# Kernel tuning notes

Measured on AMD Instinct MI355X. Metric: run time of the kernel, lower is better.

Reference implementation:

```python
import jax, jax.numpy as jnp
import numpy as np

C = 128
K = 5
M = 150000   # num vertices
NF = 300000  # num faces
D = 192      # volume side
NEG_SLOPE = 0.2


def _x_shift(K):
    # Exactly replicates the torch module's grid construction.
    grid = np.linspace(-K // 2, K // 2, K)
    grid_3d = np.stack(np.meshgrid(grid, grid, grid), axis=0).transpose(2, 1, 3, 0)
    return jnp.asarray(grid_3d.reshape(-1, 3), jnp.float32)  # [K^3, 3]


def _trilinear_border(vol, g):
    # vol: [D1, D2, D3]; g: [N, 3] normalized coords in (x, y, z) order
    # (x -> D3/W, y -> D2/H, z -> D1/D), align_corners=True, padding_mode='border'.
    D1, D2, D3 = vol.shape
    def pix(c, S):
        return jnp.clip((c + 1.0) * 0.5 * (S - 1), 0.0, S - 1.0)
    ix, iy, iz = pix(g[:, 0], D3), pix(g[:, 1], D2), pix(g[:, 2], D1)
    x0f, y0f, z0f = jnp.floor(ix), jnp.floor(iy), jnp.floor(iz)
    wx, wy, wz = ix - x0f, iy - y0f, iz - z0f
    x0 = x0f.astype(jnp.int32); y0 = y0f.astype(jnp.int32); z0 = z0f.astype(jnp.int32)
    x1 = jnp.minimum(x0 + 1, D3 - 1)
    y1 = jnp.minimum(y0 + 1, D2 - 1)
    z1 = jnp.minimum(z0 + 1, D1 - 1)
    c000 = vol[z0, y0, x0]; c001 = vol[z0, y0, x1]
    c010 = vol[z0, y1, x0]; c011 = vol[z0, y1, x1]
    c100 = vol[z1, y0, x0]; c101 = vol[z1, y0, x1]
    c110 = vol[z1, y1, x0]; c111 = vol[z1, y1, x1]
    c00 = c000 * (1 - wx) + c001 * wx
    c01 = c010 * (1 - wx) + c011 * wx
    c10 = c100 * (1 - wx) + c101 * wx
    c11 = c110 * (1 - wx) + c111 * wx
    c0 = c00 * (1 - wy) + c01 * wy
    c1 = c10 * (1 - wy) + c11 * wy
    return c0 * (1 - wz) + c1 * wz


def _leaky(x):
    return jnp.where(x >= 0, x, NEG_SLOPE * x)


def setup_inputs() -> dict:
    key = jax.random.key(0)
    ks = jax.random.split(key, 9)
    v = jax.random.uniform(ks[0], (1, M, 3), jnp.float32, -0.9, 0.9)
    f = jax.random.randint(ks[1], (1, NF, 3), 0, M, jnp.int32)
    V = jax.random.normal(ks[2], (1, 1, D, D, D), jnp.float32)
    def init(k, shape, fan):
        return jax.random.normal(k, shape, jnp.float32) / np.sqrt(fan).astype(np.float32)
    Wconv = init(ks[3], (C, 1, K, K, K), K ** 3)
    bconv = jnp.zeros((C,), jnp.float32)
    Wlfc = init(ks[4], (C, C), C)
    blfc = jnp.zeros((C,), jnp.float32)
    W1 = init(ks[5], (C, 6), 6)
    b1 = jnp.zeros((C,), jnp.float32)
    W2 = init(ks[6], (4 * C, 2 * C), 2 * C)
    b2 = jnp.zeros((4 * C,), jnp.float32)
    W3 = init(ks[7], (2 * C, 4 * C), 4 * C)
    b3 = jnp.zeros((2 * C,), jnp.float32)
    return dict(v=v, f=f, V=V, Wconv=Wconv, bconv=bconv, Wlfc=Wlfc, blfc=blfc,
                W1=W1, b1=b1, W2=W2, b2=b2, W3=W3, b3=b3)


def reference(v, f, V, Wconv, bconv, Wlfc, blfc, W1, b1, W2, b2, W3, b3):
    m = v.shape[1]
    D1, D2, D3 = V.shape[2], V.shape[3], V.shape[4]
    Dm = max(D1, D2, D3)
    rescale = jnp.array([D3 / Dm, D2 / Dm, D1 / Dm], jnp.float32)
    x_shift = _x_shift(K)  # [K^3, 3]

    # --- cube sampling (Q = n_scale = 1), done under no_grad in torch ---
    pts = (v[0][:, None, :] + x_shift / Dm * 2.0) / rescale  # [m, K^3, 3]
    cubes = _trilinear_border(V[0, 0], pts.reshape(-1, 3)).reshape(m, K ** 3)
    cubes = jax.lax.stop_gradient(cubes)

    # --- localconv: Conv3d with full-size kernel == GEMM over flattened cube ---
    z_local = cubes @ Wconv.reshape(C, -1).T + bconv      # [m, C]
    z_local = _leaky(z_local)
    z_local = _leaky(z_local @ Wlfc.T + blfc)             # [m, C]

    # --- vertex normals (area-weighted face-normal accumulation, pytorch3d style) ---
    faces = f[0]
    vv = v[0]
    p0, p1, p2 = vv[faces[:, 0]], vv[faces[:, 1]], vv[faces[:, 2]]
    fn = jnp.cross(p1 - p0, p2 - p0)
    vn = jnp.zeros_like(vv)
    vn = vn.at[faces[:, 0]].add(fn).at[faces[:, 1]].add(fn).at[faces[:, 2]].add(fn)
    vn = vn / jnp.maximum(jnp.linalg.norm(vn, axis=-1, keepdims=True), 1e-6)

    # --- point-wise MLP fusion ---
    x = jnp.concatenate([v, vn[None]], axis=2)            # [1, m, 6]
    z_point = _leaky(x @ W1.T + b1)                       # [1, m, C]
    z = jnp.concatenate([z_point, z_local[None]], axis=2) # [1, m, 2C]
    z = _leaky(z @ W2.T + b2)                             # [1, m, 4C]
    z = _leaky(z @ W3.T + b3)                             # [1, m, 2C]
    return z
```

## Files before the change

kernel.cpp:

```cpp
#include <hip/hip_runtime.h>
#include <hip/hip_fp16.h>

#define NEG_SLOPE 0.2f

using f16x8 = __attribute__((ext_vector_type(8))) _Float16;
using f32x4 = __attribute__((ext_vector_type(4))) float;

__device__ __forceinline__ float leakyf(float x) { return x >= 0.f ? x : NEG_SLOPE * x; }

__device__ __forceinline__ void gload_lds16(const void* g, void* l) {
    __builtin_amdgcn_global_load_lds(
        (const __attribute__((address_space(1))) unsigned int*)g,
        (__attribute__((address_space(3))) unsigned int*)l, 16, 0, 0);
}

#define MFMA16(a, b, c) __builtin_amdgcn_mfma_f32_16x16x32_f16(a, b, c, 0, 0, 0)

__global__ __launch_bounds__(256)
void normals_kernel(const float* __restrict__ v, const int* __restrict__ f,
                    float* __restrict__ vn, int nf) {
    int i = blockIdx.x * 256 + threadIdx.x;
    if (i >= nf) return;
    int i0 = f[3 * i], i1 = f[3 * i + 1], i2 = f[3 * i + 2];
    float p0x = v[3 * i0], p0y = v[3 * i0 + 1], p0z = v[3 * i0 + 2];
    float ux = v[3 * i1] - p0x, uy = v[3 * i1 + 1] - p0y, uz = v[3 * i1 + 2] - p0z;
    float wx = v[3 * i2] - p0x, wy = v[3 * i2 + 1] - p0y, wz = v[3 * i2 + 2] - p0z;
    float fx = uy * wz - uz * wy;
    float fy = uz * wx - ux * wz;
    float fz = ux * wy - uy * wx;
    atomicAdd(&vn[3 * i0 + 0], fx); atomicAdd(&vn[3 * i0 + 1], fy); atomicAdd(&vn[3 * i0 + 2], fz);
    atomicAdd(&vn[3 * i1 + 0], fx); atomicAdd(&vn[3 * i1 + 1], fy); atomicAdd(&vn[3 * i1 + 2], fz);
    atomicAdd(&vn[3 * i2 + 0], fx); atomicAdd(&vn[3 * i2 + 1], fy); atomicAdd(&vn[3 * i2 + 2], fz);
}

__global__ __launch_bounds__(256)
void code_hist_kernel(const float* __restrict__ v, int* __restrict__ codes,
                      int* __restrict__ hist, int M) {
    int i = blockIdx.x * 256 + threadIdx.x;
    if (i >= M) return;
    int cx = min(max((int)((v[3 * i + 0] + 1.f) * 8.f), 0), 15);
    int cy = min(max((int)((v[3 * i + 1] + 1.f) * 8.f), 0), 15);
    int cz = min(max((int)((v[3 * i + 2] + 1.f) * 8.f), 0), 15);
    int code = 0;
#pragma unroll
    for (int b = 0; b < 4; ++b)
        code |= (((cx >> b) & 1) << (3 * b)) | (((cy >> b) & 1) << (3 * b + 1)) |
                (((cz >> b) & 1) << (3 * b + 2));
    codes[i] = code;
    atomicAdd(&hist[code], 1);
}

__global__ __launch_bounds__(1024)
void scan_kernel(const int* __restrict__ hist, int* __restrict__ offs) {
    __shared__ int s[1024];
    int t = threadIdx.x;
    int v0 = hist[4 * t], v1 = hist[4 * t + 1], v2 = hist[4 * t + 2], v3 = hist[4 * t + 3];
    int sum = v0 + v1 + v2 + v3;
    s[t] = sum;
    __syncthreads();
    for (int d = 1; d < 1024; d <<= 1) {
        int val = (t >= d) ? s[t - d] : 0;
        __syncthreads();
        s[t] += val;
        __syncthreads();
    }
    int excl = s[t] - sum;
    offs[4 * t + 0] = excl;
    offs[4 * t + 1] = excl + v0;
    offs[4 * t + 2] = excl + v0 + v1;
    offs[4 * t + 3] = excl + v0 + v1 + v2;
}

__global__ __launch_bounds__(256)
void scatter_kernel(const int* __restrict__ codes, int* __restrict__ offs,
                    int* __restrict__ perm, int M) {
    int i = blockIdx.x * 256 + threadIdx.x;
    if (i >= M) return;
    int pos = atomicAdd(&offs[codes[i]], 1);
    perm[pos] = i;
}

__global__ __launch_bounds__(256)
void sample_kernel(const float* __restrict__ v, const float* __restrict__ vol,
                   const int* __restrict__ perm,
                   __half* __restrict__ cubes, int m_start, int cnt, int nwg) {
    __shared__ float bbox[2][392];
    __shared__ int pi0[2][16];
    __shared__ float pw[2][16];
    const int half = threadIdx.x >> 7;
    const int q = threadIdx.x & 127;
    int q8 = nwg >> 3, r8 = nwg & 7;
    int xcd = blockIdx.x & 7, idxb = blockIdx.x >> 3;
    int bid = (xcd < r8 ? xcd * (q8 + 1) : r8 * (q8 + 1) + (xcd - r8) * q8) + idxb;
    int ml = bid * 2 + half;
    bool valid = ml < cnt;
    int m = valid ? perm[m_start + ml] : 0;

    if (valid && q < 15) {
        int axis = q / 5, idx = q - 5 * axis;
        float g = -3.f + 1.25f * (float)idx;
        float p = v[3 * m + axis] + g / 192.f * 2.f;
        float pos = fminf(fmaxf((p + 1.f) * 0.5f * 191.f, 0.f), 191.f);
        float fl = floorf(pos);
        pi0[half][q] = (int)fl;
        pw[half][q] = pos - fl;
    }
    __syncthreads();
    if (valid) {
        int xlo = pi0[half][0], ylo = pi0[half][5], zlo = pi0[half][10];
        for (int i = q; i < 392; i += 128) {
            int dx = i & 7;
            int dy = (i >> 3) % 7;
            int dz = i / 56;
            int X = min(xlo + dx, 191), Y = min(ylo + dy, 191), Z = min(zlo + dz, 191);
            bbox[half][i] = vol[Z * 36864 + Y * 192 + X];
        }
    }
    __syncthreads();
    if (!valid) return;
    __half* dst = cubes + (size_t)ml * 128;
    if (q >= 125) { dst[q] = __float2half(0.f); return; }
    int a = q % 5, b = (q / 5) % 5, c = q / 25;
    int xlo = pi0[half][0], ylo = pi0[half][5], zlo = pi0[half][10];
    int gx0 = pi0[half][a], gy0 = pi0[half][5 + b], gz0 = pi0[half][10 + c];
    float wxv = pw[half][a], wyv = pw[half][5 + b], wzv = pw[half][10 + c];
    int x0 = gx0 - xlo, y0 = gy0 - ylo, z0 = gz0 - zlo;
    int x1 = min(gx0 + 1, 191) - xlo;
    int y1 = min(gy0 + 1, 191) - ylo;
    int z1 = min(gz0 + 1, 191) - zlo;
    const float* bb = bbox[half];
    int b00 = (z0 * 7 + y0) * 8, b01 = (z0 * 7 + y1) * 8;
    int b10 = (z1 * 7 + y0) * 8, b11 = (z1 * 7 + y1) * 8;
    float c000 = bb[b00 + x0], c001 = bb[b00 + x1];
    float c010 = bb[b01 + x0], c011 = bb[b01 + x1];
    float c100 = bb[b10 + x0], c101 = bb[b10 + x1];
    float c110 = bb[b11 + x0], c111 = bb[b11 + x1];
    float omx = 1.f - wxv, omy = 1.f - wyv, omz = 1.f - wzv;
    float c00 = c000 * omx + c001 * wxv;
    float c01 = c010 * omx + c011 * wxv;
    float c10 = c100 * omx + c101 * wxv;
    float c11 = c110 * omx + c111 * wxv;
    float c0 = c00 * omy + c01 * wyv;
    float c1 = c10 * omy + c11 * wyv;
    dst[25 * a + 5 * b + c] = __float2half(c0 * omz + c1 * wzv);
}

__global__ __launch_bounds__(256)
void prep_weights(const float* __restrict__ Wconv, const float* __restrict__ Wlfc,
                  const float* __restrict__ W2, const float* __restrict__ W3,
                  __half* __restrict__ wpadh, __half* __restrict__ wlfch,
                  __half* __restrict__ w2h, __half* __restrict__ w3h) {
    int b = blockIdx.x, t = threadIdx.x;
    if (b < 64) {
        int i = b * 256 + t; int ch = i >> 7, k = i & 127;
        wpadh[i] = __float2half(k < 125 ? Wconv[ch * 125 + k] : 0.f);
    } else if (b < 128) {
        int i = (b - 64) * 256 + t; wlfch[i] = __float2half(Wlfc[i]);
    } else if (b < 640) {
        int i = (b - 128) * 256 + t; w2h[i] = __float2half(W2[i]);
    } else {
        int i = (b - 640) * 256 + t; w3h[i] = __float2half(W3[i]);
    }
}

__global__ __launch_bounds__(256)
void point_kernel(const float* __restrict__ v, const float* __restrict__ vn,
                  const int* __restrict__ perm,
                  const float* __restrict__ W1, const float* __restrict__ b1,
                  __half* __restrict__ zcat, int m_start, int cnt) {
    int ml = blockIdx.x * 2 + (threadIdx.x >> 7);
    if (ml >= cnt) return;
    int n = threadIdx.x & 127;
    int m = perm[m_start + ml];
    float x0 = v[3 * m], x1 = v[3 * m + 1], x2 = v[3 * m + 2];
    float nx = vn[3 * m], ny = vn[3 * m + 1], nz = vn[3 * m + 2];
    float nrm = fmaxf(sqrtf(nx * nx + ny * ny + nz * nz), 1e-6f);
    nx /= nrm; ny /= nrm; nz /= nrm;
    const float* w = W1 + n * 6;
    float z = b1[n] + x0 * w[0] + x1 * w[1] + x2 * w[2] + nx * w[3] + ny * w[4] + nz * w[5];
    zcat[(size_t)ml * 256 + n] = __float2half(leakyf(z));
}

__global__ __launch_bounds__(256)
void convlfc_kernel(const __half* __restrict__ cubes, const __half* __restrict__ wconvh,
                    const float* __restrict__ bconv, const __half* __restrict__ wlfch,
                    const float* __restrict__ blfc, __half* __restrict__ zcat) {
    __shared__ __half Zt[128 * 128];
    __shared__ __half As[128 * 64];
    __shared__ __half Bs[128 * 64];
    const int t = threadIdx.x;
    const int lane = t & 63, wave = t >> 6;
    const int lr = lane & 15, lg = lane >> 4;
    const int wm = wave >> 1, wn = wave & 1;
    const int m0 = blockIdx.x * 128;
    const int srow = t >> 3;
    const int scb = ((t & 7) << 4) ^ (((t >> 3) & 7) << 4);
    const int swz = (lr & 7) << 4;

    const __half* Ag = cubes + (size_t)(m0 + srow) * 128 + (scb >> 1);
    const __half* Bg = wconvh + (size_t)srow * 128 + (scb >> 1);
    __half* Al = As + wave * 512;
    __half* Bl = Bs + wave * 512;
    const char* aB = (const char*)As + (wm * 64 + lr) * 128;
    const char* bB = (const char*)Bs + (wn * 64 + lr) * 128;

    f32x4 acc[4][4] = {};
    for (int kc = 0; kc < 128; kc += 64) {
#pragma unroll
        for (int i = 0; i < 4; ++i) {
            gload_lds16(Ag + (size_t)i * 32 * 128 + kc, Al + i * 2048);
            gload_lds16(Bg + (size_t)i * 32 * 128 + kc, Bl + i * 2048);
        }
        __syncthreads();
#pragma unroll
        for (int kk = 0; kk < 2; ++kk) {
            const int ko = (kk * 64 + lg * 16) ^ swz;
            f16x8 af[4], bf[4];
#pragma unroll
            for (int fx = 0; fx < 4; ++fx) {
                af[fx] = *(const f16x8*)(aB + fx * 2048 + ko);
                bf[fx] = *(const f16x8*)(bB + fx * 2048 + ko);
            }
#pragma unroll
            for (int fm = 0; fm < 4; ++fm)
#pragma unroll
                for (int fn = 0; fn < 4; ++fn)
                    acc[fm][fn] = MFMA16(af[fm], bf[fn], acc[fm][fn]);
        }
        __syncthreads();
    }
#pragma unroll
    for (int fm = 0; fm < 4; ++fm) {
#pragma unroll
        for (int fn = 0; fn < 4; ++fn) {
            int col = wn * 64 + fn * 16 + lr;
            float bias = bconv[col];
#pragma unroll
            for (int r = 0; r < 4; ++r) {
                int row = wm * 64 + fm * 16 + lg * 4 + r;
                float val = leakyf(acc[fm][fn][r] + bias);
                *(__half*)((char*)Zt + row * 256 + ((2 * col) ^ ((row & 7) << 4))) = __float2half(val);
            }
        }
    }
    __syncthreads();

    const __half* Bg2 = wlfch + (size_t)srow * 128 + (scb >> 1);
    const char* zR = (const char*)Zt + (wm * 64 + lr) * 256;
    f32x4 acc2[4][4] = {};
    for (int kc = 0; kc < 128; kc += 64) {
#pragma unroll
        for (int i = 0; i < 4; ++i)
            gload_lds16(Bg2 + (size_t)i * 32 * 128 + kc, Bl + i * 2048);
        __syncthreads();
#pragma unroll
        for (int kk = 0; kk < 2; ++kk) {
            const int kb = kc * 2 + kk * 64 + lg * 16;
            const int ko = (kk * 64 + lg * 16) ^ swz;
            f16x8 af[4], bf[4];
#pragma unroll
            for (int fx = 0; fx < 4; ++fx) {
                af[fx] = *(const f16x8*)(zR + fx * 4096 + (kb ^ swz));
                bf[fx] = *(const f16x8*)(bB + fx * 2048 + ko);
            }
#pragma unroll
            for (int fm = 0; fm < 4; ++fm)
#pragma unroll
                for (int fn = 0; fn < 4; ++fn)
                    acc2[fm][fn] = MFMA16(af[fm], bf[fn], acc2[fm][fn]);
        }
        __syncthreads();
    }
#pragma unroll
    for (int fm = 0; fm < 4; ++fm) {
#pragma unroll
        for (int fn = 0; fn < 4; ++fn) {
            int col = wn * 64 + fn * 16 + lr;
            float bias = blfc[col];
#pragma unroll
            for (int r = 0; r < 4; ++r) {
                int row = m0 + wm * 64 + fm * 16 + lg * 4 + r;
                zcat[(size_t)row * 256 + 128 + col] = __float2half(leakyf(acc2[fm][fn][r] + bias));
            }
        }
    }
}

template<bool F32OUT>
__global__ __launch_bounds__(256)
void gemm_mfma(const __half* __restrict__ A, const __half* __restrict__ W,
               const float* __restrict__ bias, void* __restrict__ outp,
               int K, int Meff, int OS, int OC, const int* __restrict__ rowmap) {
    __shared__ __half As[8192];
    __shared__ __half Bs[8192];
    const int t = threadIdx.x;
    const int lane = t & 63, wave = t >> 6;
    const int lr = lane & 15, lg = lane >> 4;
    const int wm = wave >> 1, wn = wave & 1;
    const int m0 = blockIdx.x * 128, n0 = blockIdx.y * 128;

    const int srow = t >> 3;
    const int scb = ((t & 7) << 4) ^ (((t >> 3) & 7) << 4);
    const __half* Ag = A + (size_t)(m0 + srow) * K + (scb >> 1);
    const __half* Wg = W + (size_t)(n0 + srow) * K + (scb >> 1);
    __half* Al = As + wave * 512;
    __half* Bl = Bs + wave * 512;

    const int swz = (lr & 7) << 4;
    const char* aB = (const char*)As + (wm * 64 + lr) * 128;
    const char* bB = (const char*)Bs + (wn * 64 + lr) * 128;
    const int k0 = (lg * 16) ^ swz;
    const int k1 = (64 + lg * 16) ^ swz;

    f32x4 acc[4][4] = {};

    for (int kc = 0; kc < K; kc += 64) {
#pragma unroll
        for (int i = 0; i < 4; ++i) {
            gload_lds16(Ag + (size_t)i * 32 * K + kc, Al + i * 2048);
            gload_lds16(Wg + (size_t)i * 32 * K + kc, Bl + i * 2048);
        }
        __syncthreads();
        f16x8 af[4], bf[4];
#pragma unroll
        for (int fx = 0; fx < 4; ++fx) {
            af[fx] = *(const f16x8*)(aB + fx * 2048 + k0);
            bf[fx] = *(const f16x8*)(bB + fx * 2048 + k0);
        }
#pragma unroll
        for (int fm = 0; fm < 4; ++fm)
#pragma unroll
            for (int fn = 0; fn < 4; ++fn)
                acc[fm][fn] = MFMA16(af[fm], bf[fn], acc[fm][fn]);
#pragma unroll
        for (int fx = 0; fx < 4; ++fx) {
            af[fx] = *(const f16x8*)(aB + fx * 2048 + k1);
            bf[fx] = *(const f16x8*)(bB + fx * 2048 + k1);
        }
#pragma unroll
        for (int fm = 0; fm < 4; ++fm)
#pragma unroll
            for (int fn = 0; fn < 4; ++fn)
                acc[fm][fn] = MFMA16(af[fm], bf[fn], acc[fm][fn]);
        __syncthreads();
    }

    float bv[4];
#pragma unroll
    for (int fn = 0; fn < 4; ++fn) bv[fn] = bias[n0 + wn * 64 + fn * 16 + lr];
    const int rbase = m0 + wm * 64 + lg * 4;
    const int cbase = OC + n0 + wn * 64 + lr;
#pragma unroll
    for (int fm = 0; fm < 4; ++fm) {
#pragma unroll
        for (int r = 0; r < 4; ++r) {
            int row = rbase + fm * 16 + r;
            if (row < Meff) {
                size_t orow = (size_t)(rowmap ? rowmap[row] : row);
#pragma unroll
                for (int fn = 0; fn < 4; ++fn) {
                    float val = leakyf(acc[fm][fn][r] + bv[fn]);
                    if (F32OUT)
                        ((float*)outp)[orow * OS + cbase + fn * 16] = val;
                    else
                        ((__half*)outp)[orow * OS + cbase + fn * 16] = __float2half(val);
                }
            }
        }
    }
}

extern "C" void kernel_launch(void* const* d_in, const int* in_sizes, int n_in,
                              void* d_out, int out_size, void* d_ws, size_t ws_size,
                              hipStream_t stream) {
    const float* v = (const float*)d_in[0];
    const int* f = (const int*)d_in[1];
    const float* vol = (const float*)d_in[2];
    const float* Wconv = (const float*)d_in[3];
    const float* bconv = (const float*)d_in[4];
    const float* Wlfc = (const float*)d_in[5];
    const float* blfc = (const float*)d_in[6];
    const float* W1 = (const float*)d_in[7];
    const float* b1 = (const float*)d_in[8];
    const float* W2 = (const float*)d_in[9];
    const float* b2 = (const float*)d_in[10];
    const float* W3 = (const float*)d_in[11];
    const float* b3 = (const float*)d_in[12];
    float* out = (float*)d_out;
    const int M = in_sizes[0] / 3;
    const int NF = in_sizes[1] / 3;

    char* base = (char*)d_ws;
    float* vn = (float*)base;
    size_t off = ((size_t)M * 12 + 255) & ~(size_t)255;
    int* codes = (int*)(base + off); off += ((size_t)M * 4 + 255) & ~(size_t)255;
    int* perm  = (int*)(base + off); off += ((size_t)M * 4 + 255) & ~(size_t)255;
    int* hist  = (int*)(base + off); off += 4096 * 4;
    int* offs  = (int*)(base + off); off += 4096 * 4;
    __half* wpadh = (__half*)(base + off); off += 32768;
    __half* wlfch = (__half*)(base + off); off += 32768;
    __half* w2h = (__half*)(base + off); off += 262144;
    __half* w3h = (__half*)(base + off); off += 262144;
    size_t avail = ws_size > off ? ws_size - off : 0;
    size_t Mpad = ((size_t)M + 127) & ~(size_t)127;
    size_t chm = (avail / 1792) & ~(size_t)127;
    if (chm > Mpad) chm = Mpad;
    if (chm < 128) chm = 128;
    __half* cubes = (__half*)(base + off);
    __half* zcat = cubes + chm * 128;
    __half* h = zcat + chm * 256;

    hipMemsetAsync(vn, 0, (size_t)M * 12, stream);
    hipMemsetAsync(hist, 0, 4096 * 4, stream);
    normals_kernel<<<(NF + 255) / 256, 256, 0, stream>>>(v, f, vn, NF);
    code_hist_kernel<<<(M + 255) / 256, 256, 0, stream>>>(v, codes, hist, M);
    scan_kernel<<<1, 1024, 0, stream>>>(hist, offs);
    scatter_kernel<<<(M + 255) / 256, 256, 0, stream>>>(codes, offs, perm, M);
    prep_weights<<<1152, 256, 0, stream>>>(Wconv, Wlfc, W2, W3, wpadh, wlfch, w2h, w3h);

    for (size_t ms = 0; ms < (size_t)M; ms += chm) {
        size_t rem = (size_t)M - ms;
        int cnt = (int)(rem < chm ? rem : chm);
        int mb = (cnt + 127) / 128;
        int nblk = (cnt + 1) / 2;
        sample_kernel<<<nblk, 256, 0, stream>>>(v, vol, perm, cubes, (int)ms, cnt, nblk);
        convlfc_kernel<<<mb, 256, 0, stream>>>(cubes, wpadh, bconv, wlfch, blfc, zcat);
        point_kernel<<<(cnt + 1) / 2, 256, 0, stream>>>(v, vn, perm, W1, b1, zcat, (int)ms, cnt);
        gemm_mfma<false><<<dim3(mb, 4), 256, 0, stream>>>(zcat, w2h, b2, h, 256, mb * 128, 512, 0, nullptr);
        gemm_mfma<true><<<dim3(mb, 2), 256, 0, stream>>>(h, w3h, b3, out, 512, cnt, 256, 0, perm + ms);
    }
}
```

Before: 560.3 us.

## Replace global atomic normal scatter with counting-sort and LDS accumulation

Face normals are first written to a per-face buffer. Face-vertex incidences are then counting-sorted into 256-vertex bins through a per-block histogram, a scan and a scatter. A gather kernel accumulates each bin's normals with shared-memory atomics and writes vn directly, so the memset and the millions of contended global float atomics go away. In exchange it adds four extra launches, a serial single-block scan and extra workspace, which may shrink the chunk size left for the main pipeline.

```diff
diff --git a/kernel.cpp b/kernel.cpp
--- a/kernel.cpp
+++ b/kernel.cpp
@@ -17,20 +17,106 @@
 #define MFMA16(a, b, c) __builtin_amdgcn_mfma_f32_16x16x32_f16(a, b, c, 0, 0, 0)
 
 __global__ __launch_bounds__(256)
-void normals_kernel(const float* __restrict__ v, const int* __restrict__ f,
-                    float* __restrict__ vn, int nf) {
+void fn_kernel(const float* __restrict__ v, const int* __restrict__ f,
+               float4* __restrict__ fn4, int nf) {
     int i = blockIdx.x * 256 + threadIdx.x;
     if (i >= nf) return;
     int i0 = f[3 * i], i1 = f[3 * i + 1], i2 = f[3 * i + 2];
     float p0x = v[3 * i0], p0y = v[3 * i0 + 1], p0z = v[3 * i0 + 2];
     float ux = v[3 * i1] - p0x, uy = v[3 * i1 + 1] - p0y, uz = v[3 * i1 + 2] - p0z;
     float wx = v[3 * i2] - p0x, wy = v[3 * i2 + 1] - p0y, wz = v[3 * i2 + 2] - p0z;
-    float fx = uy * wz - uz * wy;
-    float fy = uz * wx - ux * wz;
-    float fz = ux * wy - uy * wx;
-    atomicAdd(&vn[3 * i0 + 0], fx); atomicAdd(&vn[3 * i0 + 1], fy); atomicAdd(&vn[3 * i0 + 2], fz);
-    atomicAdd(&vn[3 * i1 + 0], fx); atomicAdd(&vn[3 * i1 + 1], fy); atomicAdd(&vn[3 * i1 + 2], fz);
-    atomicAdd(&vn[3 * i2 + 0], fx); atomicAdd(&vn[3 * i2 + 1], fy); atomicAdd(&vn[3 * i2 + 2], fz);
+    fn4[i] = make_float4(uy * wz - uz * wy, uz * wx - ux * wz, ux * wy - uy * wx, 0.f);
+}
+
+__global__ __launch_bounds__(256)
+void inc_hist_kernel(const int* __restrict__ f, unsigned* __restrict__ gh,
+                     int NE, int NB) {
+    __shared__ unsigned h[1024];
+    const int t = threadIdx.x, blk = blockIdx.x;
+    h[t] = 0; h[t + 256] = 0; h[t + 512] = 0; h[t + 768] = 0;
+    __syncthreads();
+    int base = blk * 4096;
+#pragma unroll
+    for (int k = 0; k < 16; ++k) {
+        int idx = base + k * 256 + t;
+        if (idx < NE) atomicAdd(&h[((unsigned)f[idx]) >> 8], 1u);
+    }
+    __syncthreads();
+#pragma unroll
+    for (int k = 0; k < 4; ++k) { int b = t + k * 256; gh[(size_t)b * NB + blk] = h[b]; }
+}
+
+__global__ __launch_bounds__(1024)
+void inc_scan_kernel(unsigned* __restrict__ gh, unsigned* __restrict__ binstart, int NB) {
+    __shared__ unsigned s[1024];
+    const int t = threadIdx.x;
+    unsigned sum = 0;
+    for (int r = 0; r < NB; ++r) sum += gh[(size_t)t * NB + r];
+    s[t] = sum;
+    __syncthreads();
+    for (int d = 1; d < 1024; d <<= 1) {
+        unsigned val = (t >= d) ? s[t - d] : 0;
+        __syncthreads();
+        s[t] += val;
+        __syncthreads();
+    }
+    unsigned base = s[t] - sum;
+    binstart[t] = base;
+    if (t == 1023) binstart[1024] = s[t];
+    unsigned run = base;
+    for (int r = 0; r < NB; ++r) {
+        unsigned c = gh[(size_t)t * NB + r];
+        gh[(size_t)t * NB + r] = run;
+        run += c;
+    }
+}
+
+__global__ __launch_bounds__(256)
+void inc_scatter_kernel(const int* __restrict__ f, const unsigned* __restrict__ gh,
+                        unsigned* __restrict__ sortedV, unsigned* __restrict__ sortedE,
+                        int NE, int NB) {
+    __shared__ unsigned loc[1024];
+    const int t = threadIdx.x, blk = blockIdx.x;
+#pragma unroll
+    for (int k = 0; k < 4; ++k) { int b = t + k * 256; loc[b] = gh[(size_t)b * NB + blk]; }
+    __syncthreads();
+    int base = blk * 4096;
+#pragma unroll
+    for (int k = 0; k < 16; ++k) {
+        int idx = base + k * 256 + t;
+        if (idx < NE) {
+            unsigned vv = (unsigned)f[idx];
+            unsigned pos = atomicAdd(&loc[vv >> 8], 1u);
+            sortedV[pos] = vv;
+            sortedE[pos] = (unsigned)idx;
+        }
+    }
+}
+
+__global__ __launch_bounds__(256)
+void vn_gather_kernel(const unsigned* __restrict__ sortedV, const unsigned* __restrict__ sortedE,
+                      const float4* __restrict__ fn4, const unsigned* __restrict__ binstart,
+                      float* __restrict__ vn, int M) {
+    __shared__ float acc[768];
+    const int t = threadIdx.x, b = blockIdx.x;
+    acc[t] = 0.f; acc[t + 256] = 0.f; acc[t + 512] = 0.f;
+    __syncthreads();
+    unsigned s = binstart[b], e = binstart[b + 1];
+    for (unsigned i = s + t; i < e; i += 256) {
+        unsigned vv = sortedV[i];
+        float4 fn = fn4[sortedE[i] / 3];
+        int lv = (int)(vv & 255u) * 3;
+        atomicAdd(&acc[lv + 0], fn.x);
+        atomicAdd(&acc[lv + 1], fn.y);
+        atomicAdd(&acc[lv + 2], fn.z);
+    }
+    __syncthreads();
+    int gv = b * 256 + t;
+    if (gv < M) {
+        vn[3 * gv + 0] = acc[t * 3 + 0];
+        vn[3 * gv + 1] = acc[t * 3 + 1];
+        vn[3 * gv + 2] = acc[t * 3 + 2];
+    }
 }
 
 __global__ __launch_bounds__(256)
@@ -389,6 +475,8 @@
     float* out = (float*)d_out;
     const int M = in_sizes[0] / 3;
     const int NF = in_sizes[1] / 3;
+    const int NE = 3 * NF;
+    const int NB = (NE + 4095) / 4096;
 
     char* base = (char*)d_ws;
     float* vn = (float*)base;
@@ -397,6 +485,11 @@
     int* perm  = (int*)(base + off); off += ((size_t)M * 4 + 255) & ~(size_t)255;
     int* hist  = (int*)(base + off); off += 4096 * 4;
     int* offs  = (int*)(base + off); off += 4096 * 4;
+    float4* fn4 = (float4*)(base + off); off += (size_t)NF * 16;
+    unsigned* sortedV = (unsigned*)(base + off); off += ((size_t)NE * 4 + 255) & ~(size_t)255;
+    unsigned* sortedE = (unsigned*)(base + off); off += ((size_t)NE * 4 + 255) & ~(size_t)255;
+    unsigned* gh = (unsigned*)(base + off); off += ((size_t)1024 * NB * 4 + 255) & ~(size_t)255;
+    unsigned* binstart = (unsigned*)(base + off); off += 1032 * 4;
     __half* wpadh = (__half*)(base + off); off += 32768;
     __half* wlfch = (__half*)(base + off); off += 32768;
     __half* w2h = (__half*)(base + off); off += 262144;
@@ -410,9 +503,13 @@
     __half* zcat = cubes + chm * 128;
     __half* h = zcat + chm * 256;
 
-    hipMemsetAsync(vn, 0, (size_t)M * 12, stream);
+    fn_kernel<<<(NF + 255) / 256, 256, 0, stream>>>(v, f, fn4, NF);
+    inc_hist_kernel<<<NB, 256, 0, stream>>>(f, gh, NE, NB);
+    inc_scan_kernel<<<1, 1024, 0, stream>>>(gh, binstart, NB);
+    inc_scatter_kernel<<<NB, 256, 0, stream>>>(f, gh, sortedV, sortedE, NE, NB);
+    vn_gather_kernel<<<(M + 255) / 256, 256, 0, stream>>>(sortedV, sortedE, fn4, binstart, vn, M);
+
     hipMemsetAsync(hist, 0, 4096 * 4, stream);
-    normals_kernel<<<(NF + 255) / 256, 256, 0, stream>>>(v, f, vn, NF);
     code_hist_kernel<<<(M + 255) / 256, 256, 0, stream>>>(v, codes, hist, M);
     scan_kernel<<<1, 1024, 0, stream>>>(hist, offs);
     scatter_kernel<<<(M + 255) / 256, 256, 0, stream>>>(codes, offs, perm, M);
```

Result: slower. 870.1 us (+55.3%).
